# Performance work log

Hardware: AMD Instinct MI355X
Metric: run time of the kernel (lower is better)

Reference implementation:

```python
import jax, jax.numpy as jnp
import numpy as np

B, C, N, T = 16, 32, 1024, 128
R = 10  # low-rank bottleneck of W1/W2


def setup_inputs() -> dict:
    key = jax.random.key(0)
    k1, k2, k3, k4 = jax.random.split(key, 4)
    x = jax.random.normal(k1, (B, C, N, T), dtype=jnp.float32)
    W1 = jax.random.normal(k2, (R, N), dtype=jnp.float32) * 0.05
    W2 = jax.random.normal(k3, (R, N), dtype=jnp.float32) * 0.05
    alpha = jax.random.normal(k4, (C,), dtype=jnp.float32) * 0.1
    return {"x": x, "W1": W1, "W2": W2, "alpha": alpha}


def reference(x, W1, W2, alpha):
    # k = q = einsum('bint,i->btn', x, alpha): contract channels -> [B, T, N]
    k = jnp.einsum('bcnt,c->btn', x, alpha)
    # low-rank bilinear scores: (k @ W1^T) @ (k @ W2^T)^T -> [B, T, T]
    kw1 = jnp.einsum('btn,rn->btr', k, W1)   # [B, T, R]
    qw2 = jnp.einsum('btn,rn->btr', k, W2)   # [B, T, R]
    scores = jnp.einsum('btr,bsr->bts', kw1, qw2)  # [B, T, T]
    att = jax.nn.softmax(scores, axis=-1)
    # weighted sum over time: einsum('bti,bcni->bcnt', att, x)
    return jnp.einsum('bts,bcns->bcnt', att, x)
```

## Files before the change

### kernel.cpp

```cpp
#include <hip/hip_runtime.h>
#include <hip/hip_bf16.h>


#define B_ 16
#define C_ 32
#define N_ 1024
#define T_ 128
#define R_ 10
#define CH_ 16
#define NCH_ (N_ / CH_)

typedef __bf16 bf16x8 __attribute__((ext_vector_type(8)));
typedef __bf16 bf16x4 __attribute__((ext_vector_type(4)));
typedef float f32x4 __attribute__((ext_vector_type(4)));

__global__ __launch_bounds__(256) void k_reduce_c(const float* __restrict__ x,
                                                  const float* __restrict__ alpha,
                                                  float* __restrict__ k) {
    int bid = blockIdx.x;
    int b   = bid >> 7;
    int nc  = bid & 127;
    int tid = threadIdx.x;
    int nl  = tid >> 5;
    int lc  = tid & 31;
    int n   = nc * 8 + nl;
    const float4* xb = reinterpret_cast<const float4*>(
        x + ((size_t)(b * C_) * N_ + n) * T_) + lc;
    float4 acc = {0.f, 0.f, 0.f, 0.f};
    #pragma unroll 8
    for (int c = 0; c < C_; ++c) {
        float a = alpha[c];
        float4 v = xb[(size_t)c * (N_ * T_ / 4)];
        acc.x += a * v.x; acc.y += a * v.y; acc.z += a * v.z; acc.w += a * v.w;
    }
    reinterpret_cast<float4*>(k + ((size_t)b * N_ + n) * T_)[lc] = acc;
}

__global__ __launch_bounds__(128) void kw_partial(const float* __restrict__ k,
                                                  const float* __restrict__ W1,
                                                  const float* __restrict__ W2,
                                                  float* __restrict__ p1,
                                                  float* __restrict__ p2) {
    __shared__ __align__(16) float ws[NCH_][20];
    int bid = blockIdx.x;
    int b   = bid >> 4;
    int ch  = bid & (CH_ - 1);
    int n0  = ch * NCH_;
    int t   = threadIdx.x;
    for (int i = t; i < NCH_ * R_; i += 128) {
        int r = i / NCH_, nl = i % NCH_;
        ws[nl][r]      = W1[r * N_ + n0 + nl];
        ws[nl][R_ + r] = W2[r * N_ + n0 + nl];
    }
    __syncthreads();
    float a1[R_] = {}, a2[R_] = {};
    const float* kb = k + ((size_t)b * N_ + n0) * T_ + t;
    for (int nl = 0; nl < NCH_; ++nl) {
        float kv = kb[nl * T_];
        float wv[20];
        const float4* wr = reinterpret_cast<const float4*>(&ws[nl][0]);
        #pragma unroll
        for (int q = 0; q < 5; ++q) *reinterpret_cast<float4*>(&wv[q * 4]) = wr[q];
        #pragma unroll
        for (int r = 0; r < R_; ++r) {
            a1[r] += kv * wv[r];
            a2[r] += kv * wv[R_ + r];
        }
    }
    size_t o = ((size_t)(b * CH_ + ch) * T_ + t) * R_;
    #pragma unroll
    for (int r = 0; r < R_; ++r) { p1[o + r] = a1[r]; p2[o + r] = a2[r]; }
}

__global__ __launch_bounds__(128) void scores_softmax(const float* __restrict__ p1,
                                                      const float* __restrict__ p2,
                                                      __bf16* __restrict__ att) {
    __shared__ __align__(16) float kw1s[T_][12];
    __shared__ __align__(16) float kw2s[T_][12];
    __shared__ float sc[T_][T_ + 1];
    int b = blockIdx.x;
    int t = threadIdx.x;
    #pragma unroll
    for (int r = 0; r < R_; ++r) {
        float s1 = 0.f, s2 = 0.f;
        for (int ch = 0; ch < CH_; ++ch) {
            size_t o = ((size_t)(b * CH_ + ch) * T_ + t) * R_ + r;
            s1 += p1[o]; s2 += p2[o];
        }
        kw1s[t][r] = s1; kw2s[t][r] = s2;
    }
    __syncthreads();
    float myw[R_];
    #pragma unroll
    for (int r = 0; r < R_; ++r) myw[r] = kw1s[t][r];
    float mx = -1e30f;
    for (int s = 0; s < T_; ++s) {
        float wv[12];
        const float4* qr = reinterpret_cast<const float4*>(&kw2s[s][0]);
        #pragma unroll
        for (int q = 0; q < 3; ++q) *reinterpret_cast<float4*>(&wv[q * 4]) = qr[q];
        float v = 0.f;
        #pragma unroll
        for (int r = 0; r < R_; ++r) v += myw[r] * wv[r];
        sc[t][s] = v;
        mx = fmaxf(mx, v);
    }
    float sum = 0.f;
    for (int s = 0; s < T_; ++s) {
        float e = __expf(sc[t][s] - mx);
        sc[t][s] = e;
        sum += e;
    }
    float inv = 1.0f / sum;
    __bf16* arow = att + ((size_t)b * T_ + t) * T_;
    for (int s8 = 0; s8 < T_; s8 += 8) {
        bf16x8 h;
        #pragma unroll
        for (int q = 0; q < 8; ++q) h[q] = (__bf16)(sc[t][s8 + q] * inv);
        *reinterpret_cast<bf16x8*>(arow + s8) = h;
    }
}

__global__ __launch_bounds__(256) void out_gemm(const float* __restrict__ x,
                                                const __bf16* __restrict__ att,
                                                float* __restrict__ out) {
    __shared__ __align__(16) __bf16 attl[T_][T_];
    __shared__ __align__(16) __bf16 xsl[64][T_];
    int bid = blockIdx.x;
    int nc  = bid & 15;
    int c   = (bid >> 4) & 31;
    int b   = bid >> 9;
    int tid = threadIdx.x;
    size_t slab = ((size_t)(b * C_ + c) * N_ + nc * 64) * T_;
    char* attb = reinterpret_cast<char*>(&attl[0][0]);
    char* xb   = reinterpret_cast<char*>(&xsl[0][0]);

    const uint4* ga = reinterpret_cast<const uint4*>(att + (size_t)b * T_ * T_);
    #pragma unroll
    for (int i = 0; i < 8; ++i) {
        int e   = i * 256 + tid;
        int row = e >> 4;
        int bc  = ((e & 15) * 16) ^ ((row & 7) << 4);
        *reinterpret_cast<uint4*>(attb + row * 256 + bc) = ga[e];
    }
    const float4* gx = reinterpret_cast<const float4*>(x + slab);
    #pragma unroll
    for (int i = 0; i < 8; ++i) {
        int e   = i * 256 + tid;
        int row = e >> 5;
        float4 v = gx[e];
        bf16x4 h = {(__bf16)v.x, (__bf16)v.y, (__bf16)v.z, (__bf16)v.w};
        int bc = ((e & 31) * 8) ^ ((row & 7) << 4);
        *reinterpret_cast<bf16x4*>(xb + row * 256 + bc) = h;
    }
    __syncthreads();

    int wave = tid >> 6, lane = tid & 63;
    int r16 = lane & 15, g = lane >> 4;
    int wt = wave & 1, wn = wave >> 1;
    int swz = (r16 & 7) << 4;
    f32x4 acc[2][4] = {};
    #pragma unroll
    for (int ks = 0; ks < 4; ++ks) {
        int kc = ks * 64 + g * 16;
        bf16x8 a[4], bx[2];
        #pragma unroll
        for (int tt = 0; tt < 4; ++tt) {
            int row = wt * 64 + tt * 16 + r16;
            a[tt] = *reinterpret_cast<const bf16x8*>(attb + row * 256 + (kc ^ swz));
        }
        #pragma unroll
        for (int nn = 0; nn < 2; ++nn) {
            int row = wn * 32 + nn * 16 + r16;
            bx[nn] = *reinterpret_cast<const bf16x8*>(xb + row * 256 + (kc ^ swz));
        }
        #pragma unroll
        for (int nn = 0; nn < 2; ++nn)
            #pragma unroll
            for (int tt = 0; tt < 4; ++tt)
                acc[nn][tt] = __builtin_amdgcn_mfma_f32_16x16x32_bf16(
                    a[tt], bx[nn], acc[nn][tt], 0, 0, 0);
    }
    float* o = out + slab;
    #pragma unroll
    for (int nn = 0; nn < 2; ++nn) {
        int n_l = wn * 32 + nn * 16 + r16;
        #pragma unroll
        for (int tt = 0; tt < 4; ++tt) {
            int t_l = wt * 64 + tt * 16 + g * 4;
            *reinterpret_cast<f32x4*>(o + (size_t)n_l * T_ + t_l) = acc[nn][tt];
        }
    }
}

extern "C" void kernel_launch(void* const* d_in, const int* in_sizes, int n_in,
                              void* d_out, int out_size, void* d_ws, size_t ws_size,
                              hipStream_t stream) {
    const float* x     = (const float*)d_in[0];
    const float* W1    = (const float*)d_in[1];
    const float* W2    = (const float*)d_in[2];
    const float* alpha = (const float*)d_in[3];
    float* out = (float*)d_out;

    float* k  = (float*)d_ws;
    float* p1 = k + (size_t)B_ * N_ * T_;
    float* p2 = p1 + (size_t)B_ * CH_ * T_ * R_;
    __bf16* att = (__bf16*)(p2 + (size_t)B_ * CH_ * T_ * R_);

    k_reduce_c<<<dim3(B_ * (N_ / 8)), dim3(256), 0, stream>>>(x, alpha, k);
    kw_partial<<<dim3(B_ * CH_), dim3(128), 0, stream>>>(k, W1, W2, p1, p2);
    scores_softmax<<<dim3(B_), dim3(128), 0, stream>>>(p1, p2, att);
    out_gemm<<<dim3(B_ * C_ * (N_ / 64)), dim3(256), 0, stream>>>(x, att, out);
}
```

Before: 190.4 us.

## Fuse channel reduction and bf16 cast of x, pipeline output GEMM over slabs

A new first kernel reads x once and does three jobs: it reduces over channels, computes the low-rank projection partials, and writes a swizzled bf16 copy of x into the workspace. The output GEMM then streams that bf16 copy instead of re-reading and converting fp32 x. Each GEMM block handles 8 slabs with double-buffered LDS prefetch and keeps the attention tile loaded across them. This removes the k intermediate and one launch, but adds a 128MB bf16 write. The fused kernel also runs far fewer blocks, and the new path is only taken when the workspace is large enough.

```diff
diff --git a/kernel.cpp b/kernel.cpp
--- a/kernel.cpp
+++ b/kernel.cpp
@@ -13,19 +13,220 @@
 typedef __bf16 bf16x8 __attribute__((ext_vector_type(8)));
 typedef __bf16 bf16x4 __attribute__((ext_vector_type(4)));
 typedef float f32x4 __attribute__((ext_vector_type(4)));
+typedef float f32x2 __attribute__((ext_vector_type(2)));
+
+__global__ __launch_bounds__(256) void k_cast_kw(const float* __restrict__ x,
+                                                 const float* __restrict__ W1,
+                                                 const float* __restrict__ W2,
+                                                 const float* __restrict__ alpha,
+                                                 __bf16* __restrict__ xb16,
+                                                 float* __restrict__ p1,
+                                                 float* __restrict__ p2) {
+    __shared__ float klds[64][T_];
+    __shared__ __align__(16) float wl[64][24];
+    int bid = blockIdx.x;
+    int h   = bid & 1;
+    int nc  = (bid >> 1) & 15;
+    int b   = bid >> 5;
+    int n0  = nc * 64, c0 = h * 16;
+    int tid = threadIdx.x;
+
+    for (int i = tid; i < 64 * 20; i += 256) {
+        int nl = i & 63, q = i >> 6;
+        wl[nl][q < 10 ? q : q + 2] =
+            (q < 10) ? W1[q * N_ + n0 + nl] : W2[(q - 10) * N_ + n0 + nl];
+    }
+    float al[16];
+    #pragma unroll
+    for (int c = 0; c < 16; ++c) al[c] = alpha[c0 + c];
+
+    int col = tid & 31;
+    f32x4 acc[8] = {};
+    const float* xbase = x + (((size_t)b * C_ + c0) * N_ + n0) * T_;
+    #pragma unroll 2
+    for (int cc = 0; cc < 16; ++cc) {
+        const float4* gx = reinterpret_cast<const float4*>(xbase + (size_t)cc * N_ * T_);
+        char* xw = (char*)xb16 + (((size_t)(b * C_ + c0 + cc) * 16 + nc) * 16384);
+        #pragma unroll
+        for (int j = 0; j < 8; ++j) {
+            float4 v = gx[tid + j * 256];
+            int row = (tid >> 5) + j * 8;
+            float a = al[cc];
+            acc[j][0] += a * v.x; acc[j][1] += a * v.y;
+            acc[j][2] += a * v.z; acc[j][3] += a * v.w;
+            bf16x4 hv = {(__bf16)v.x, (__bf16)v.y, (__bf16)v.z, (__bf16)v.w};
+            *reinterpret_cast<bf16x4*>(xw + row * 256 + ((col * 8) ^ ((row & 7) << 4))) = hv;
+        }
+    }
+    #pragma unroll
+    for (int j = 0; j < 8; ++j) {
+        int row = (tid >> 5) + j * 8;
+        *reinterpret_cast<f32x4*>(&klds[row][col * 4]) = acc[j];
+    }
+    __syncthreads();
+    int t = tid & 127, rg = tid >> 7;
+    float a[10] = {};
+    #pragma unroll 4
+    for (int n = 0; n < 64; ++n) {
+        float kv = klds[n][t];
+        const float* wr = &wl[n][rg * 12];
+        f32x4 wA = *reinterpret_cast<const f32x4*>(wr);
+        f32x4 wB = *reinterpret_cast<const f32x4*>(wr + 4);
+        f32x2 wC = *reinterpret_cast<const f32x2*>(wr + 8);
+        a[0] += kv * wA[0]; a[1] += kv * wA[1]; a[2] += kv * wA[2]; a[3] += kv * wA[3];
+        a[4] += kv * wB[0]; a[5] += kv * wB[1]; a[6] += kv * wB[2]; a[7] += kv * wB[3];
+        a[8] += kv * wC[0]; a[9] += kv * wC[1];
+    }
+    float* pd = (rg ? p2 : p1) + (((size_t)b * 32 + (bid & 31)) * T_ + t) * R_;
+    #pragma unroll
+    for (int q = 0; q < 5; ++q) {
+        f32x2 v = {a[2 * q], a[2 * q + 1]};
+        *reinterpret_cast<f32x2*>(pd + 2 * q) = v;
+    }
+}
+
+__global__ __launch_bounds__(128) void scores_softmax32(const float* __restrict__ p1,
+                                                        const float* __restrict__ p2,
+                                                        __bf16* __restrict__ att) {
+    __shared__ __align__(16) float kw1s[T_][12];
+    __shared__ __align__(16) float kw2s[T_][12];
+    __shared__ float sc[T_][T_ + 1];
+    int b = blockIdx.x;
+    int t = threadIdx.x;
+    #pragma unroll
+    for (int r = 0; r < R_; ++r) {
+        float s1 = 0.f, s2 = 0.f;
+        for (int ch = 0; ch < 32; ++ch) {
+            size_t o = (((size_t)b * 32 + ch) * T_ + t) * R_ + r;
+            s1 += p1[o]; s2 += p2[o];
+        }
+        kw1s[t][r] = s1; kw2s[t][r] = s2;
+    }
+    __syncthreads();
+    float myw[R_];
+    #pragma unroll
+    for (int r = 0; r < R_; ++r) myw[r] = kw1s[t][r];
+    float mx = -1e30f;
+    for (int s = 0; s < T_; ++s) {
+        float wv[12];
+        const float4* qr = reinterpret_cast<const float4*>(&kw2s[s][0]);
+        #pragma unroll
+        for (int q = 0; q < 3; ++q) *reinterpret_cast<float4*>(&wv[q * 4]) = qr[q];
+        float v = 0.f;
+        #pragma unroll
+        for (int r = 0; r < R_; ++r) v += myw[r] * wv[r];
+        sc[t][s] = v;
+        mx = fmaxf(mx, v);
+    }
+    float sum = 0.f;
+    for (int s = 0; s < T_; ++s) {
+        float e = __expf(sc[t][s] - mx);
+        sc[t][s] = e;
+        sum += e;
+    }
+    float inv = 1.0f / sum;
+    __bf16* arow = att + ((size_t)b * T_ + t) * T_;
+    for (int s8 = 0; s8 < T_; s8 += 8) {
+        bf16x8 hv;
+        #pragma unroll
+        for (int q = 0; q < 8; ++q) hv[q] = (__bf16)(sc[t][s8 + q] * inv);
+        *reinterpret_cast<bf16x8*>(arow + s8) = hv;
+    }
+}
+
+__global__ __launch_bounds__(256) void out_gemm_p(const __bf16* __restrict__ xb16,
+                                                  const __bf16* __restrict__ att,
+                                                  float* __restrict__ out) {
+    __shared__ __align__(16) __bf16 attl[T_][T_];
+    __shared__ __align__(16) __bf16 xbuf[2][64][T_];
+    int bid = blockIdx.x;
+    int b = bid >> 6, j = bid & 63;
+    int tid = threadIdx.x;
+    char* attb = (char*)&attl[0][0];
+
+    const uint4* ga = reinterpret_cast<const uint4*>(att + (size_t)b * T_ * T_);
+    uint4 ar[8];
+    #pragma unroll
+    for (int i = 0; i < 8; ++i) ar[i] = ga[i * 256 + tid];
+    const uint4* gx0 = reinterpret_cast<const uint4*>(xb16) + ((size_t)b * 512 + (size_t)j * 8) * 1024;
+    uint4 xr[4];
+    #pragma unroll
+    for (int q = 0; q < 4; ++q) xr[q] = gx0[q * 256 + tid];
+    #pragma unroll
+    for (int i = 0; i < 8; ++i) {
+        int e = i * 256 + tid, row = e >> 4;
+        int bc = ((e & 15) * 16) ^ ((row & 7) << 4);
+        *reinterpret_cast<uint4*>(attb + row * 256 + bc) = ar[i];
+    }
+    {
+        uint4* lb = reinterpret_cast<uint4*>(&xbuf[0][0][0]);
+        #pragma unroll
+        for (int q = 0; q < 4; ++q) lb[q * 256 + tid] = xr[q];
+    }
+    __syncthreads();
+
+    int wave = tid >> 6, lane = tid & 63;
+    int r16 = lane & 15, g = lane >> 4;
+    int wt = wave & 1, wn = wave >> 1;
+    int swz = (r16 & 7) << 4;
+
+    for (int i = 0; i < 8; ++i) {
+        int cur = i & 1;
+        uint4 nx[4];
+        if (i < 7) {
+            const uint4* gx = reinterpret_cast<const uint4*>(xb16) +
+                              ((size_t)b * 512 + (size_t)j * 8 + i + 1) * 1024;
+            #pragma unroll
+            for (int q = 0; q < 4; ++q) nx[q] = gx[q * 256 + tid];
+        }
+        const char* xb = (const char*)&xbuf[cur][0][0];
+        f32x4 acc[2][4] = {};
+        #pragma unroll
+        for (int ks = 0; ks < 4; ++ks) {
+            int kc = ks * 64 + g * 16;
+            bf16x8 a[4], bx[2];
+            #pragma unroll
+            for (int tt = 0; tt < 4; ++tt)
+                a[tt] = *reinterpret_cast<const bf16x8*>(
+                    attb + (wt * 64 + tt * 16 + r16) * 256 + (kc ^ swz));
+            #pragma unroll
+            for (int nn = 0; nn < 2; ++nn)
+                bx[nn] = *reinterpret_cast<const bf16x8*>(
+                    xb + (wn * 32 + nn * 16 + r16) * 256 + (kc ^ swz));
+            #pragma unroll
+            for (int nn = 0; nn < 2; ++nn)
+                #pragma unroll
+                for (int tt = 0; tt < 4; ++tt)
+                    acc[nn][tt] = __builtin_amdgcn_mfma_f32_16x16x32_bf16(
+                        a[tt], bx[nn], acc[nn][tt], 0, 0, 0);
+        }
+        int sid = j * 8 + i;
+        float* o = out + (((size_t)(b * C_ + (sid >> 4))) * N_ + (sid & 15) * 64) * T_;
+        #pragma unroll
+        for (int nn = 0; nn < 2; ++nn) {
+            int n_l = wn * 32 + nn * 16 + r16;
+            #pragma unroll
+            for (int tt = 0; tt < 4; ++tt)
+                *reinterpret_cast<f32x4*>(o + (size_t)n_l * T_ + (wt * 64 + tt * 16 + g * 4)) = acc[nn][tt];
+        }
+        if (i < 7) {
+            uint4* lb = reinterpret_cast<uint4*>(&xbuf[cur ^ 1][0][0]);
+            #pragma unroll
+            for (int q = 0; q < 4; ++q) lb[q * 256 + tid] = nx[q];
+        }
+        __syncthreads();
+    }
+}
 
 __global__ __launch_bounds__(256) void k_reduce_c(const float* __restrict__ x,
                                                   const float* __restrict__ alpha,
                                                   float* __restrict__ k) {
     int bid = blockIdx.x;
-    int b   = bid >> 7;
-    int nc  = bid & 127;
+    int b = bid >> 7, nc = bid & 127;
     int tid = threadIdx.x;
-    int nl  = tid >> 5;
-    int lc  = tid & 31;
-    int n   = nc * 8 + nl;
-    const float4* xb = reinterpret_cast<const float4*>(
-        x + ((size_t)(b * C_) * N_ + n) * T_) + lc;
+    int nl = tid >> 5, lc = tid & 31;
+    int n = nc * 8 + nl;
+    const float4* xb = reinterpret_cast<const float4*>(x + ((size_t)(b * C_) * N_ + n) * T_) + lc;
     float4 acc = {0.f, 0.f, 0.f, 0.f};
     #pragma unroll 8
     for (int c = 0; c < C_; ++c) {
@@ -43,28 +244,24 @@
                                                   float* __restrict__ p2) {
     __shared__ __align__(16) float ws[NCH_][20];
     int bid = blockIdx.x;
-    int b   = bid >> 4;
-    int ch  = bid & (CH_ - 1);
-    int n0  = ch * NCH_;
-    int t   = threadIdx.x;
+    int b = bid >> 4, ch = bid & (CH_ - 1);
+    int n0 = ch * NCH_;
+    int t = threadIdx.x;
     for (int i = t; i < NCH_ * R_; i += 128) {
         int r = i / NCH_, nl = i % NCH_;
-        ws[nl][r]      = W1[r * N_ + n0 + nl];
+        ws[nl][r] = W1[r * N_ + n0 + nl];
         ws[nl][R_ + r] = W2[r * N_ + n0 + nl];
     }
     __syncthreads();
     float a1[R_] = {}, a2[R_] = {};
     const float* kb = k + ((size_t)b * N_ + n0) * T_ + t;
+    #pragma unroll 4
     for (int nl = 0; nl < NCH_; ++nl) {
         float kv = kb[nl * T_];
-        float wv[20];
-        const float4* wr = reinterpret_cast<const float4*>(&ws[nl][0]);
-        #pragma unroll
-        for (int q = 0; q < 5; ++q) *reinterpret_cast<float4*>(&wv[q * 4]) = wr[q];
         #pragma unroll
         for (int r = 0; r < R_; ++r) {
-            a1[r] += kv * wv[r];
-            a2[r] += kv * wv[R_ + r];
+            a1[r] += kv * ws[nl][r];
+            a2[r] += kv * ws[nl][R_ + r];
         }
     }
     size_t o = ((size_t)(b * CH_ + ch) * T_ + t) * R_;
@@ -72,9 +269,9 @@
     for (int r = 0; r < R_; ++r) { p1[o + r] = a1[r]; p2[o + r] = a2[r]; }
 }
 
-__global__ __launch_bounds__(128) void scores_softmax(const float* __restrict__ p1,
-                                                      const float* __restrict__ p2,
-                                                      __bf16* __restrict__ att) {
+__global__ __launch_bounds__(128) void scores_softmax16(const float* __restrict__ p1,
+                                                        const float* __restrict__ p2,
+                                                        __bf16* __restrict__ att) {
     __shared__ __align__(16) float kw1s[T_][12];
     __shared__ __align__(16) float kw2s[T_][12];
     __shared__ float sc[T_][T_ + 1];
@@ -95,13 +292,9 @@
     for (int r = 0; r < R_; ++r) myw[r] = kw1s[t][r];
     float mx = -1e30f;
     for (int s = 0; s < T_; ++s) {
-        float wv[12];
-        const float4* qr = reinterpret_cast<const float4*>(&kw2s[s][0]);
-        #pragma unroll
-        for (int q = 0; q < 3; ++q) *reinterpret_cast<float4*>(&wv[q * 4]) = qr[q];
         float v = 0.f;
         #pragma unroll
-        for (int r = 0; r < R_; ++r) v += myw[r] * wv[r];
+        for (int r = 0; r < R_; ++r) v += myw[r] * kw2s[s][r];
         sc[t][s] = v;
         mx = fmaxf(mx, v);
     }
@@ -114,10 +307,10 @@
     float inv = 1.0f / sum;
     __bf16* arow = att + ((size_t)b * T_ + t) * T_;
     for (int s8 = 0; s8 < T_; s8 += 8) {
-        bf16x8 h;
-        #pragma unroll
-        for (int q = 0; q < 8; ++q) h[q] = (__bf16)(sc[t][s8 + q] * inv);
-        *reinterpret_cast<bf16x8*>(arow + s8) = h;
+        bf16x8 hv;
+        #pragma unroll
+        for (int q = 0; q < 8; ++q) hv[q] = (__bf16)(sc[t][s8 + q] * inv);
+        *reinterpret_cast<bf16x8*>(arow + s8) = hv;
     }
 }
 
@@ -127,34 +320,28 @@
     __shared__ __align__(16) __bf16 attl[T_][T_];
     __shared__ __align__(16) __bf16 xsl[64][T_];
     int bid = blockIdx.x;
-    int nc  = bid & 15;
-    int c   = (bid >> 4) & 31;
-    int b   = bid >> 9;
+    int nc = bid & 15, c = (bid >> 4) & 31, b = bid >> 9;
     int tid = threadIdx.x;
     size_t slab = ((size_t)(b * C_ + c) * N_ + nc * 64) * T_;
     char* attb = reinterpret_cast<char*>(&attl[0][0]);
-    char* xb   = reinterpret_cast<char*>(&xsl[0][0]);
-
+    char* xb = reinterpret_cast<char*>(&xsl[0][0]);
     const uint4* ga = reinterpret_cast<const uint4*>(att + (size_t)b * T_ * T_);
     #pragma unroll
     for (int i = 0; i < 8; ++i) {
-        int e   = i * 256 + tid;
-        int row = e >> 4;
-        int bc  = ((e & 15) * 16) ^ ((row & 7) << 4);
+        int e = i * 256 + tid, row = e >> 4;
+        int bc = ((e & 15) * 16) ^ ((row & 7) << 4);
         *reinterpret_cast<uint4*>(attb + row * 256 + bc) = ga[e];
     }
     const float4* gx = reinterpret_cast<const float4*>(x + slab);
     #pragma unroll
     for (int i = 0; i < 8; ++i) {
-        int e   = i * 256 + tid;
-        int row = e >> 5;
+        int e = i * 256 + tid, row = e >> 5;
         float4 v = gx[e];
-        bf16x4 h = {(__bf16)v.x, (__bf16)v.y, (__bf16)v.z, (__bf16)v.w};
+        bf16x4 hv = {(__bf16)v.x, (__bf16)v.y, (__bf16)v.z, (__bf16)v.w};
         int bc = ((e & 31) * 8) ^ ((row & 7) << 4);
-        *reinterpret_cast<bf16x4*>(xb + row * 256 + bc) = h;
-    }
-    __syncthreads();
-
+        *reinterpret_cast<bf16x4*>(xb + row * 256 + bc) = hv;
+    }
+    __syncthreads();
     int wave = tid >> 6, lane = tid & 63;
     int r16 = lane & 15, g = lane >> 4;
     int wt = wave & 1, wn = wave >> 1;
@@ -165,31 +352,24 @@
         int kc = ks * 64 + g * 16;
         bf16x8 a[4], bx[2];
         #pragma unroll
-        for (int tt = 0; tt < 4; ++tt) {
-            int row = wt * 64 + tt * 16 + r16;
-            a[tt] = *reinterpret_cast<const bf16x8*>(attb + row * 256 + (kc ^ swz));
-        }
-        #pragma unroll
-        for (int nn = 0; nn < 2; ++nn) {
-            int row = wn * 32 + nn * 16 + r16;
-            bx[nn] = *reinterpret_cast<const bf16x8*>(xb + row * 256 + (kc ^ swz));
-        }
+        for (int tt = 0; tt < 4; ++tt)
+            a[tt] = *reinterpret_cast<const bf16x8*>(attb + (wt * 64 + tt * 16 + r16) * 256 + (kc ^ swz));
         #pragma unroll
         for (int nn = 0; nn < 2; ++nn)
+            bx[nn] = *reinterpret_cast<const bf16x8*>(xb + (wn * 32 + nn * 16 + r16) * 256 + (kc ^ swz));
+        #pragma unroll
+        for (int nn = 0; nn < 2; ++nn)
             #pragma unroll
             for (int tt = 0; tt < 4; ++tt)
-                acc[nn][tt] = __builtin_amdgcn_mfma_f32_16x16x32_bf16(
-                    a[tt], bx[nn], acc[nn][tt], 0, 0, 0);
+                acc[nn][tt] = __builtin_amdgcn_mfma_f32_16x16x32_bf16(a[tt], bx[nn], acc[nn][tt], 0, 0, 0);
     }
     float* o = out + slab;
     #pragma unroll
     for (int nn = 0; nn < 2; ++nn) {
         int n_l = wn * 32 + nn * 16 + r16;
         #pragma unroll
-        for (int tt = 0; tt < 4; ++tt) {
-            int t_l = wt * 64 + tt * 16 + g * 4;
-            *reinterpret_cast<f32x4*>(o + (size_t)n_l * T_ + t_l) = acc[nn][tt];
-        }
+        for (int tt = 0; tt < 4; ++tt)
+            *reinterpret_cast<f32x4*>(o + (size_t)n_l * T_ + (wt * 64 + tt * 16 + g * 4)) = acc[nn][tt];
     }
 }
 
@@ -202,13 +382,24 @@
     const float* alpha = (const float*)d_in[3];
     float* out = (float*)d_out;
 
-    float* k  = (float*)d_ws;
-    float* p1 = k + (size_t)B_ * N_ * T_;
-    float* p2 = p1 + (size_t)B_ * CH_ * T_ * R_;
-    __bf16* att = (__bf16*)(p2 + (size_t)B_ * CH_ * T_ * R_);
-
-    k_reduce_c<<<dim3(B_ * (N_ / 8)), dim3(256), 0, stream>>>(x, alpha, k);
-    kw_partial<<<dim3(B_ * CH_), dim3(128), 0, stream>>>(k, W1, W2, p1, p2);
-    scores_softmax<<<dim3(B_), dim3(128), 0, stream>>>(p1, p2, att);
-    out_gemm<<<dim3(B_ * C_ * (N_ / 64)), dim3(256), 0, stream>>>(x, att, out);
-}
+    const size_t XB16 = 134217728;
+    const size_t PSZ  = 2621440;
+    if (ws_size >= XB16 + 2 * PSZ + 524288) {
+        __bf16* xb16 = (__bf16*)d_ws;
+        float* p1 = (float*)((char*)d_ws + XB16);
+        float* p2 = (float*)((char*)d_ws + XB16 + PSZ);
+        __bf16* att = (__bf16*)((char*)d_ws + XB16 + 2 * PSZ);
+        k_cast_kw<<<dim3(B_ * 32), dim3(256), 0, stream>>>(x, W1, W2, alpha, xb16, p1, p2);
+        scores_softmax32<<<dim3(B_), dim3(128), 0, stream>>>(p1, p2, att);
+        out_gemm_p<<<dim3(B_ * 64), dim3(256), 0, stream>>>(xb16, att, out);
+    } else {
+        float* k  = (float*)d_ws;
+        float* p1 = k + (size_t)B_ * N_ * T_;
+        float* p2 = p1 + (size_t)B_ * CH_ * T_ * R_;
+        __bf16* att = (__bf16*)(p2 + (size_t)B_ * CH_ * T_ * R_);
+        k_reduce_c<<<dim3(B_ * (N_ / 8)), dim3(256), 0, stream>>>(x, alpha, k);
+        kw_partial<<<dim3(B_ * CH_), dim3(128), 0, stream>>>(k, W1, W2, p1, p2);
+        scores_softmax16<<<dim3(B_), dim3(128), 0, stream>>>(p1, p2, att);
+        out_gemm<<<dim3(B_ * C_ * (N_ / 64)), dim3(256), 0, stream>>>(x, att, out);
+    }
+}
```

Measured after the change: 215.6 us. +13.2%, slower.

## Fuse scores/softmax into output GEMM and split low-rank projection reduction

Applied to the files above, without the earlier changes.

Every output GEMM block now recomputes its batch's scores and softmax in shared memory from the reduced low-rank projections, so the bf16 attention matrix no longer goes through global memory and the 16-block scores_softmax kernel (with its single-block-per-batch serial tail) is gone. Normalisation is deferred to the GEMM epilogue by scaling with 1/sum. The projection partials are split into 32 chunks with a coalesced layout and summed by a separate reduce kernel. The cost is redundant score computation across the 512 blocks per batch, plus extra shared-memory and register pressure in the GEMM kernel.

```diff
diff --git a/kernel.cpp b/kernel.cpp
--- a/kernel.cpp
+++ b/kernel.cpp
@@ -7,12 +7,11 @@
 #define N_ 1024
 #define T_ 128
 #define R_ 10
-#define CH_ 16
-#define NCH_ (N_ / CH_)
 
 typedef __bf16 bf16x8 __attribute__((ext_vector_type(8)));
 typedef __bf16 bf16x4 __attribute__((ext_vector_type(4)));
 typedef float f32x4 __attribute__((ext_vector_type(4)));
+typedef float f32x2 __attribute__((ext_vector_type(2)));
 
 __global__ __launch_bounds__(256) void k_reduce_c(const float* __restrict__ x,
                                                   const float* __restrict__ alpha,
@@ -36,122 +35,148 @@
     reinterpret_cast<float4*>(k + ((size_t)b * N_ + n) * T_)[lc] = acc;
 }
 
-__global__ __launch_bounds__(128) void kw_partial(const float* __restrict__ k,
-                                                  const float* __restrict__ W1,
-                                                  const float* __restrict__ W2,
-                                                  float* __restrict__ p1,
-                                                  float* __restrict__ p2) {
-    __shared__ __align__(16) float ws[NCH_][20];
-    int bid = blockIdx.x;
-    int b   = bid >> 4;
-    int ch  = bid & (CH_ - 1);
-    int n0  = ch * NCH_;
+__global__ __launch_bounds__(128) void kw_partial2(const float* __restrict__ k,
+                                                   const float* __restrict__ W1,
+                                                   const float* __restrict__ W2,
+                                                   float* __restrict__ p1,
+                                                   float* __restrict__ p2) {
+    __shared__ float wl[32][20];
+    int bid = blockIdx.x;
+    int b   = bid >> 5;
+    int ch  = bid & 31;
+    int n0  = ch * 32;
     int t   = threadIdx.x;
-    for (int i = t; i < NCH_ * R_; i += 128) {
-        int r = i / NCH_, nl = i % NCH_;
-        ws[nl][r]      = W1[r * N_ + n0 + nl];
-        ws[nl][R_ + r] = W2[r * N_ + n0 + nl];
+    for (int i = t; i < 32 * 20; i += 128) {
+        int nl = i & 31, q = i >> 5;
+        wl[nl][q] = (q < 10) ? W1[q * N_ + n0 + nl] : W2[(q - 10) * N_ + n0 + nl];
     }
     __syncthreads();
     float a1[R_] = {}, a2[R_] = {};
     const float* kb = k + ((size_t)b * N_ + n0) * T_ + t;
-    for (int nl = 0; nl < NCH_; ++nl) {
-        float kv = kb[nl * T_];
-        float wv[20];
-        const float4* wr = reinterpret_cast<const float4*>(&ws[nl][0]);
-        #pragma unroll
-        for (int q = 0; q < 5; ++q) *reinterpret_cast<float4*>(&wv[q * 4]) = wr[q];
-        #pragma unroll
-        for (int r = 0; r < R_; ++r) {
-            a1[r] += kv * wv[r];
-            a2[r] += kv * wv[R_ + r];
+    #pragma unroll 2
+    for (int g = 0; g < 4; ++g) {
+        float kv[8];
+        #pragma unroll
+        for (int j = 0; j < 8; ++j) kv[j] = kb[(g * 8 + j) * T_];
+        #pragma unroll
+        for (int j = 0; j < 8; ++j) {
+            int nl = g * 8 + j;
+            #pragma unroll
+            for (int r = 0; r < R_; ++r) {
+                a1[r] += kv[j] * wl[nl][r];
+                a2[r] += kv[j] * wl[nl][10 + r];
+            }
         }
     }
-    size_t o = ((size_t)(b * CH_ + ch) * T_ + t) * R_;
-    #pragma unroll
-    for (int r = 0; r < R_; ++r) { p1[o + r] = a1[r]; p2[o + r] = a2[r]; }
-}
-
-__global__ __launch_bounds__(128) void scores_softmax(const float* __restrict__ p1,
-                                                      const float* __restrict__ p2,
-                                                      __bf16* __restrict__ att) {
-    __shared__ __align__(16) float kw1s[T_][12];
-    __shared__ __align__(16) float kw2s[T_][12];
-    __shared__ float sc[T_][T_ + 1];
-    int b = blockIdx.x;
+    #pragma unroll
+    for (int r = 0; r < R_; ++r) {
+        size_t o = (((size_t)b * R_ + r) * 32 + ch) * T_ + t;
+        p1[o] = a1[r];
+        p2[o] = a2[r];
+    }
+}
+
+__global__ __launch_bounds__(128) void kw_reduce(const float* __restrict__ p1,
+                                                 const float* __restrict__ p2,
+                                                 float* __restrict__ kwc) {
+    int bid = blockIdx.x;
+    int b = bid / 20;
+    int q = bid - b * 20;
+    int w = q / 10;
+    int r = q - w * 10;
     int t = threadIdx.x;
-    #pragma unroll
-    for (int r = 0; r < R_; ++r) {
-        float s1 = 0.f, s2 = 0.f;
-        for (int ch = 0; ch < CH_; ++ch) {
-            size_t o = ((size_t)(b * CH_ + ch) * T_ + t) * R_ + r;
-            s1 += p1[o]; s2 += p2[o];
-        }
-        kw1s[t][r] = s1; kw2s[t][r] = s2;
-    }
-    __syncthreads();
-    float myw[R_];
-    #pragma unroll
-    for (int r = 0; r < R_; ++r) myw[r] = kw1s[t][r];
-    float mx = -1e30f;
-    for (int s = 0; s < T_; ++s) {
-        float wv[12];
-        const float4* qr = reinterpret_cast<const float4*>(&kw2s[s][0]);
-        #pragma unroll
-        for (int q = 0; q < 3; ++q) *reinterpret_cast<float4*>(&wv[q * 4]) = qr[q];
-        float v = 0.f;
-        #pragma unroll
-        for (int r = 0; r < R_; ++r) v += myw[r] * wv[r];
-        sc[t][s] = v;
-        mx = fmaxf(mx, v);
-    }
-    float sum = 0.f;
-    for (int s = 0; s < T_; ++s) {
-        float e = __expf(sc[t][s] - mx);
-        sc[t][s] = e;
-        sum += e;
-    }
-    float inv = 1.0f / sum;
-    __bf16* arow = att + ((size_t)b * T_ + t) * T_;
-    for (int s8 = 0; s8 < T_; s8 += 8) {
-        bf16x8 h;
-        #pragma unroll
-        for (int q = 0; q < 8; ++q) h[q] = (__bf16)(sc[t][s8 + q] * inv);
-        *reinterpret_cast<bf16x8*>(arow + s8) = h;
-    }
-}
-
-__global__ __launch_bounds__(256) void out_gemm(const float* __restrict__ x,
-                                                const __bf16* __restrict__ att,
-                                                float* __restrict__ out) {
+    const float* src = (w ? p2 : p1) + (((size_t)b * R_ + r) * 32) * T_ + t;
+    float s = 0.f;
+    #pragma unroll
+    for (int ch = 0; ch < 32; ++ch) s += src[ch * T_];
+    kwc[(((size_t)b * 2 + w) * R_ + r) * T_ + t] = s;
+}
+
+__global__ __launch_bounds__(256) void softmax_gemm(const float* __restrict__ x,
+                                                    const float* __restrict__ kwc,
+                                                    float* __restrict__ out) {
     __shared__ __align__(16) __bf16 attl[T_][T_];
     __shared__ __align__(16) __bf16 xsl[64][T_];
+    __shared__ float invs[T_];
     int bid = blockIdx.x;
     int nc  = bid & 15;
     int c   = (bid >> 4) & 31;
     int b   = bid >> 9;
     int tid = threadIdx.x;
     size_t slab = ((size_t)(b * C_ + c) * N_ + nc * 64) * T_;
-    char* attb = reinterpret_cast<char*>(&attl[0][0]);
-    char* xb   = reinterpret_cast<char*>(&xsl[0][0]);
-
-    const uint4* ga = reinterpret_cast<const uint4*>(att + (size_t)b * T_ * T_);
+    char*  attb = (char*)&attl[0][0];
+    float* kws  = (float*)&xsl[0][0];
+
+    const float* kb = kwc + (size_t)b * 2560;
+    float kwreg[10];
+    #pragma unroll
+    for (int i = 0; i < 10; ++i) kwreg[i] = kb[i * 256 + tid];
+    const float4* gx = reinterpret_cast<const float4*>(x + slab);
+    float4 xr[8];
+    #pragma unroll
+    for (int i = 0; i < 8; ++i) xr[i] = gx[i * 256 + tid];
+    #pragma unroll
+    for (int i = 0; i < 10; ++i) {
+        int idx = i * 256 + tid;
+        int w   = idx >= 1280;
+        int rem = idx - w * 1280;
+        int r   = rem >> 7, t0 = rem & 127;
+        kws[(w * 128 + t0) * 12 + r] = kwreg[i];
+    }
+    __syncthreads();
+
+    int t = tid >> 1, h = tid & 1;
+    const float* w1r = &kws[t * 12];
+    f32x4 m1a = *reinterpret_cast<const f32x4*>(w1r);
+    f32x4 m1b = *reinterpret_cast<const f32x4*>(w1r + 4);
+    f32x2 m1c = *reinterpret_cast<const f32x2*>(w1r + 8);
+    const float* w2base = &kws[(128 + h * 64) * 12];
+    float mx = -1e30f;
+    #pragma unroll 4
+    for (int j = 0; j < 64; ++j) {
+        const float* w2 = w2base + j * 12;
+        f32x4 qa = *reinterpret_cast<const f32x4*>(w2);
+        f32x4 qb = *reinterpret_cast<const f32x4*>(w2 + 4);
+        f32x2 qc = *reinterpret_cast<const f32x2*>(w2 + 8);
+        float v = m1a[0]*qa[0]+m1a[1]*qa[1]+m1a[2]*qa[2]+m1a[3]*qa[3]
+                + m1b[0]*qb[0]+m1b[1]*qb[1]+m1b[2]*qb[2]+m1b[3]*qb[3]
+                + m1c[0]*qc[0]+m1c[1]*qc[1];
+        mx = fmaxf(mx, v);
+    }
+    mx = fmaxf(mx, __shfl_xor(mx, 1));
+    float sum = 0.f;
+    int swzt = (t & 7) << 4;
+    char* arow = attb + t * 256;
+    #pragma unroll 4
+    for (int j = 0; j < 32; ++j) {
+        float v[2];
+        #pragma unroll
+        for (int u = 0; u < 2; ++u) {
+            const float* w2 = w2base + (2 * j + u) * 12;
+            f32x4 qa = *reinterpret_cast<const f32x4*>(w2);
+            f32x4 qb = *reinterpret_cast<const f32x4*>(w2 + 4);
+            f32x2 qc = *reinterpret_cast<const f32x2*>(w2 + 8);
+            v[u] = m1a[0]*qa[0]+m1a[1]*qa[1]+m1a[2]*qa[2]+m1a[3]*qa[3]
+                 + m1b[0]*qb[0]+m1b[1]*qb[1]+m1b[2]*qb[2]+m1b[3]*qb[3]
+                 + m1c[0]*qc[0]+m1c[1]*qc[1];
+        }
+        float e0 = __expf(v[0] - mx), e1 = __expf(v[1] - mx);
+        sum += e0 + e1;
+        union { __bf16 hh[2]; unsigned u32; } cv;
+        cv.hh[0] = (__bf16)e0; cv.hh[1] = (__bf16)e1;
+        int bytec = (h * 128 + j * 4) ^ swzt;
+        *reinterpret_cast<unsigned*>(arow + bytec) = cv.u32;
+    }
+    sum += __shfl_xor(sum, 1);
+    if (h == 0) invs[t] = 1.0f / sum;
+    __syncthreads();
+
+    char* xbb = (char*)&xsl[0][0];
     #pragma unroll
     for (int i = 0; i < 8; ++i) {
-        int e   = i * 256 + tid;
-        int row = e >> 4;
-        int bc  = ((e & 15) * 16) ^ ((row & 7) << 4);
-        *reinterpret_cast<uint4*>(attb + row * 256 + bc) = ga[e];
-    }
-    const float4* gx = reinterpret_cast<const float4*>(x + slab);
-    #pragma unroll
-    for (int i = 0; i < 8; ++i) {
-        int e   = i * 256 + tid;
-        int row = e >> 5;
-        float4 v = gx[e];
-        bf16x4 h = {(__bf16)v.x, (__bf16)v.y, (__bf16)v.z, (__bf16)v.w};
-        int bc = ((e & 31) * 8) ^ ((row & 7) << 4);
-        *reinterpret_cast<bf16x4*>(xb + row * 256 + bc) = h;
+        int e = i * 256 + tid, row = e >> 5;
+        bf16x4 hv = {(__bf16)xr[i].x, (__bf16)xr[i].y, (__bf16)xr[i].z, (__bf16)xr[i].w};
+        *reinterpret_cast<bf16x4*>(xbb + row * 256 + (((e & 31) * 8) ^ ((row & 7) << 4))) = hv;
     }
     __syncthreads();
 
@@ -165,15 +190,13 @@
         int kc = ks * 64 + g * 16;
         bf16x8 a[4], bx[2];
         #pragma unroll
-        for (int tt = 0; tt < 4; ++tt) {
-            int row = wt * 64 + tt * 16 + r16;
-            a[tt] = *reinterpret_cast<const bf16x8*>(attb + row * 256 + (kc ^ swz));
-        }
-        #pragma unroll
-        for (int nn = 0; nn < 2; ++nn) {
-            int row = wn * 32 + nn * 16 + r16;
-            bx[nn] = *reinterpret_cast<const bf16x8*>(xb + row * 256 + (kc ^ swz));
-        }
+        for (int tt = 0; tt < 4; ++tt)
+            a[tt] = *reinterpret_cast<const bf16x8*>(
+                attb + (wt * 64 + tt * 16 + r16) * 256 + (kc ^ swz));
+        #pragma unroll
+        for (int nn = 0; nn < 2; ++nn)
+            bx[nn] = *reinterpret_cast<const bf16x8*>(
+                xbb + (wn * 32 + nn * 16 + r16) * 256 + (kc ^ swz));
         #pragma unroll
         for (int nn = 0; nn < 2; ++nn)
             #pragma unroll
@@ -187,8 +210,11 @@
         int n_l = wn * 32 + nn * 16 + r16;
         #pragma unroll
         for (int tt = 0; tt < 4; ++tt) {
-            int t_l = wt * 64 + tt * 16 + g * 4;
-            *reinterpret_cast<f32x4*>(o + (size_t)n_l * T_ + t_l) = acc[nn][tt];
+            int tb = wt * 64 + tt * 16 + g * 4;
+            f32x4 iv = *reinterpret_cast<const f32x4*>(&invs[tb]);
+            f32x4 vv = acc[nn][tt];
+            vv[0] *= iv[0]; vv[1] *= iv[1]; vv[2] *= iv[2]; vv[3] *= iv[3];
+            *reinterpret_cast<f32x4*>(o + (size_t)n_l * T_ + tb) = vv;
         }
     }
 }
@@ -202,13 +228,13 @@
     const float* alpha = (const float*)d_in[3];
     float* out = (float*)d_out;
 
-    float* k  = (float*)d_ws;
-    float* p1 = k + (size_t)B_ * N_ * T_;
-    float* p2 = p1 + (size_t)B_ * CH_ * T_ * R_;
-    __bf16* att = (__bf16*)(p2 + (size_t)B_ * CH_ * T_ * R_);
-
-    k_reduce_c<<<dim3(B_ * (N_ / 8)), dim3(256), 0, stream>>>(x, alpha, k);
-    kw_partial<<<dim3(B_ * CH_), dim3(128), 0, stream>>>(k, W1, W2, p1, p2);
-    scores_softmax<<<dim3(B_), dim3(128), 0, stream>>>(p1, p2, att);
-    out_gemm<<<dim3(B_ * C_ * (N_ / 64)), dim3(256), 0, stream>>>(x, att, out);
-}
+    float* k   = (float*)d_ws;
+    float* p1  = k  + (size_t)B_ * N_ * T_;
+    float* p2  = p1 + (size_t)B_ * R_ * 32 * T_;
+    float* kwc = p2 + (size_t)B_ * R_ * 32 * T_;
+
+    k_reduce_c <<<dim3(B_ * (N_ / 8)), dim3(256), 0, stream>>>(x, alpha, k);
+    kw_partial2<<<dim3(B_ * 32),       dim3(128), 0, stream>>>(k, W1, W2, p1, p2);
+    kw_reduce  <<<dim3(B_ * 20),       dim3(128), 0, stream>>>(p1, p2, kwc);
+    softmax_gemm<<<dim3(B_ * 512),     dim3(256), 0, stream>>>(x, kwc, out);
+}
```

Measured after the change: 295.2 us. 1.55x slower.

## Load x directly into MFMA registers and parallelize low-rank projection reduction

Applied to the files above, without the earlier changes.

The output GEMM stops staging the x slab through LDS and instead loads fp32 x straight from global memory into registers. It converts those values to bf16 MFMA operands and prefetches the next k-slice, which frees LDS and raises the occupancy hint. The low-rank projection now splits N into 32 chunks with coalesced partial layout. A new small kernel reduces those partials, so scores_softmax no longer serially sums strided partials. This adds a kernel launch, and the direct global loads are less coalesced than the previous staged copy.

```diff
diff --git a/kernel.cpp b/kernel.cpp
--- a/kernel.cpp
+++ b/kernel.cpp
@@ -7,8 +7,6 @@
 #define N_ 1024
 #define T_ 128
 #define R_ 10
-#define CH_ 16
-#define NCH_ (N_ / CH_)
 
 typedef __bf16 bf16x8 __attribute__((ext_vector_type(8)));
 typedef __bf16 bf16x4 __attribute__((ext_vector_type(4)));
@@ -36,58 +34,75 @@
     reinterpret_cast<float4*>(k + ((size_t)b * N_ + n) * T_)[lc] = acc;
 }
 
-__global__ __launch_bounds__(128) void kw_partial(const float* __restrict__ k,
-                                                  const float* __restrict__ W1,
-                                                  const float* __restrict__ W2,
-                                                  float* __restrict__ p1,
-                                                  float* __restrict__ p2) {
-    __shared__ __align__(16) float ws[NCH_][20];
-    int bid = blockIdx.x;
-    int b   = bid >> 4;
-    int ch  = bid & (CH_ - 1);
-    int n0  = ch * NCH_;
+__global__ __launch_bounds__(128) void kw_partial2(const float* __restrict__ k,
+                                                   const float* __restrict__ W1,
+                                                   const float* __restrict__ W2,
+                                                   float* __restrict__ p1,
+                                                   float* __restrict__ p2) {
+    __shared__ float wl[32][20];
+    int bid = blockIdx.x;
+    int b   = bid >> 5;
+    int ch  = bid & 31;
+    int n0  = ch * 32;
     int t   = threadIdx.x;
-    for (int i = t; i < NCH_ * R_; i += 128) {
-        int r = i / NCH_, nl = i % NCH_;
-        ws[nl][r]      = W1[r * N_ + n0 + nl];
-        ws[nl][R_ + r] = W2[r * N_ + n0 + nl];
+    for (int i = t; i < 32 * 20; i += 128) {
+        int nl = i & 31, q = i >> 5;
+        wl[nl][q] = (q < 10) ? W1[q * N_ + n0 + nl] : W2[(q - 10) * N_ + n0 + nl];
     }
     __syncthreads();
     float a1[R_] = {}, a2[R_] = {};
     const float* kb = k + ((size_t)b * N_ + n0) * T_ + t;
-    for (int nl = 0; nl < NCH_; ++nl) {
-        float kv = kb[nl * T_];
-        float wv[20];
-        const float4* wr = reinterpret_cast<const float4*>(&ws[nl][0]);
-        #pragma unroll
-        for (int q = 0; q < 5; ++q) *reinterpret_cast<float4*>(&wv[q * 4]) = wr[q];
-        #pragma unroll
-        for (int r = 0; r < R_; ++r) {
-            a1[r] += kv * wv[r];
-            a2[r] += kv * wv[R_ + r];
+    #pragma unroll 2
+    for (int g = 0; g < 4; ++g) {
+        float kv[8];
+        #pragma unroll
+        for (int j = 0; j < 8; ++j) kv[j] = kb[(g * 8 + j) * T_];
+        #pragma unroll
+        for (int j = 0; j < 8; ++j) {
+            int nl = g * 8 + j;
+            #pragma unroll
+            for (int r = 0; r < R_; ++r) {
+                a1[r] += kv[j] * wl[nl][r];
+                a2[r] += kv[j] * wl[nl][10 + r];
+            }
         }
     }
-    size_t o = ((size_t)(b * CH_ + ch) * T_ + t) * R_;
-    #pragma unroll
-    for (int r = 0; r < R_; ++r) { p1[o + r] = a1[r]; p2[o + r] = a2[r]; }
-}
-
-__global__ __launch_bounds__(128) void scores_softmax(const float* __restrict__ p1,
-                                                      const float* __restrict__ p2,
+    #pragma unroll
+    for (int r = 0; r < R_; ++r) {
+        size_t o = (((size_t)b * R_ + r) * 32 + ch) * T_ + t;
+        p1[o] = a1[r];
+        p2[o] = a2[r];
+    }
+}
+
+__global__ __launch_bounds__(128) void kw_reduce(const float* __restrict__ p1,
+                                                 const float* __restrict__ p2,
+                                                 float* __restrict__ kwc) {
+    int bid = blockIdx.x;
+    int b = bid / 20;
+    int q = bid - b * 20;
+    int w = q / 10;
+    int r = q - w * 10;
+    int t = threadIdx.x;
+    const float* src = (w ? p2 : p1) + (((size_t)b * R_ + r) * 32) * T_ + t;
+    float s = 0.f;
+    #pragma unroll
+    for (int ch = 0; ch < 32; ++ch) s += src[ch * T_];
+    kwc[(((size_t)b * 2 + w) * R_ + r) * T_ + t] = s;
+}
+
+__global__ __launch_bounds__(128) void scores_softmax(const float* __restrict__ kwc,
                                                       __bf16* __restrict__ att) {
     __shared__ __align__(16) float kw1s[T_][12];
     __shared__ __align__(16) float kw2s[T_][12];
     __shared__ float sc[T_][T_ + 1];
     int b = blockIdx.x;
     int t = threadIdx.x;
+    const float* kb = kwc + (size_t)b * 2 * R_ * T_;
     #pragma unroll
     for (int r = 0; r < R_; ++r) {
-        float s1 = 0.f, s2 = 0.f;
-        for (int ch = 0; ch < CH_; ++ch) {
-            size_t o = ((size_t)(b * CH_ + ch) * T_ + t) * R_ + r;
-            s1 += p1[o]; s2 += p2[o];
-        }
-        kw1s[t][r] = s1; kw2s[t][r] = s2;
+        kw1s[t][r] = kb[r * T_ + t];
+        kw2s[t][r] = kb[(R_ + r) * T_ + t];
     }
     __syncthreads();
     float myw[R_];
@@ -114,44 +129,31 @@
     float inv = 1.0f / sum;
     __bf16* arow = att + ((size_t)b * T_ + t) * T_;
     for (int s8 = 0; s8 < T_; s8 += 8) {
-        bf16x8 h;
-        #pragma unroll
-        for (int q = 0; q < 8; ++q) h[q] = (__bf16)(sc[t][s8 + q] * inv);
-        *reinterpret_cast<bf16x8*>(arow + s8) = h;
-    }
-}
-
-__global__ __launch_bounds__(256) void out_gemm(const float* __restrict__ x,
-                                                const __bf16* __restrict__ att,
-                                                float* __restrict__ out) {
+        bf16x8 hv;
+        #pragma unroll
+        for (int q = 0; q < 8; ++q) hv[q] = (__bf16)(sc[t][s8 + q] * inv);
+        *reinterpret_cast<bf16x8*>(arow + s8) = hv;
+    }
+}
+
+__global__ __launch_bounds__(256, 4) void out_gemm2(const float* __restrict__ x,
+                                                    const __bf16* __restrict__ att,
+                                                    float* __restrict__ out) {
     __shared__ __align__(16) __bf16 attl[T_][T_];
-    __shared__ __align__(16) __bf16 xsl[64][T_];
     int bid = blockIdx.x;
     int nc  = bid & 15;
     int c   = (bid >> 4) & 31;
     int b   = bid >> 9;
     int tid = threadIdx.x;
     size_t slab = ((size_t)(b * C_ + c) * N_ + nc * 64) * T_;
-    char* attb = reinterpret_cast<char*>(&attl[0][0]);
-    char* xb   = reinterpret_cast<char*>(&xsl[0][0]);
+    char* attb = (char*)&attl[0][0];
 
     const uint4* ga = reinterpret_cast<const uint4*>(att + (size_t)b * T_ * T_);
     #pragma unroll
     for (int i = 0; i < 8; ++i) {
-        int e   = i * 256 + tid;
-        int row = e >> 4;
-        int bc  = ((e & 15) * 16) ^ ((row & 7) << 4);
+        int e = i * 256 + tid, row = e >> 4;
+        int bc = ((e & 15) * 16) ^ ((row & 7) << 4);
         *reinterpret_cast<uint4*>(attb + row * 256 + bc) = ga[e];
-    }
-    const float4* gx = reinterpret_cast<const float4*>(x + slab);
-    #pragma unroll
-    for (int i = 0; i < 8; ++i) {
-        int e   = i * 256 + tid;
-        int row = e >> 5;
-        float4 v = gx[e];
-        bf16x4 h = {(__bf16)v.x, (__bf16)v.y, (__bf16)v.z, (__bf16)v.w};
-        int bc = ((e & 31) * 8) ^ ((row & 7) << 4);
-        *reinterpret_cast<bf16x4*>(xb + row * 256 + bc) = h;
     }
     __syncthreads();
 
@@ -159,37 +161,50 @@
     int r16 = lane & 15, g = lane >> 4;
     int wt = wave & 1, wn = wave >> 1;
     int swz = (r16 & 7) << 4;
+
+    const float* xr0 = x + slab + (size_t)(wn * 32 + r16) * T_ + g * 8;
+    const float* xr1 = xr0 + 16 * T_;
+
     f32x4 acc[2][4] = {};
+    float4 c0a = *reinterpret_cast<const float4*>(xr0);
+    float4 c0b = *reinterpret_cast<const float4*>(xr0 + 4);
+    float4 c1a = *reinterpret_cast<const float4*>(xr1);
+    float4 c1b = *reinterpret_cast<const float4*>(xr1 + 4);
     #pragma unroll
     for (int ks = 0; ks < 4; ++ks) {
+        float4 n0a, n0b, n1a, n1b;
+        if (ks < 3) {
+            int o = (ks + 1) * 32;
+            n0a = *reinterpret_cast<const float4*>(xr0 + o);
+            n0b = *reinterpret_cast<const float4*>(xr0 + o + 4);
+            n1a = *reinterpret_cast<const float4*>(xr1 + o);
+            n1b = *reinterpret_cast<const float4*>(xr1 + o + 4);
+        }
+        bf16x8 bx0 = {(__bf16)c0a.x, (__bf16)c0a.y, (__bf16)c0a.z, (__bf16)c0a.w,
+                      (__bf16)c0b.x, (__bf16)c0b.y, (__bf16)c0b.z, (__bf16)c0b.w};
+        bf16x8 bx1 = {(__bf16)c1a.x, (__bf16)c1a.y, (__bf16)c1a.z, (__bf16)c1a.w,
+                      (__bf16)c1b.x, (__bf16)c1b.y, (__bf16)c1b.z, (__bf16)c1b.w};
         int kc = ks * 64 + g * 16;
-        bf16x8 a[4], bx[2];
-        #pragma unroll
-        for (int tt = 0; tt < 4; ++tt) {
-            int row = wt * 64 + tt * 16 + r16;
-            a[tt] = *reinterpret_cast<const bf16x8*>(attb + row * 256 + (kc ^ swz));
-        }
-        #pragma unroll
-        for (int nn = 0; nn < 2; ++nn) {
-            int row = wn * 32 + nn * 16 + r16;
-            bx[nn] = *reinterpret_cast<const bf16x8*>(xb + row * 256 + (kc ^ swz));
-        }
-        #pragma unroll
-        for (int nn = 0; nn < 2; ++nn)
-            #pragma unroll
-            for (int tt = 0; tt < 4; ++tt)
-                acc[nn][tt] = __builtin_amdgcn_mfma_f32_16x16x32_bf16(
-                    a[tt], bx[nn], acc[nn][tt], 0, 0, 0);
+        bf16x8 a[4];
+        #pragma unroll
+        for (int tt = 0; tt < 4; ++tt)
+            a[tt] = *reinterpret_cast<const bf16x8*>(
+                attb + (wt * 64 + tt * 16 + r16) * 256 + (kc ^ swz));
+        #pragma unroll
+        for (int tt = 0; tt < 4; ++tt)
+            acc[0][tt] = __builtin_amdgcn_mfma_f32_16x16x32_bf16(a[tt], bx0, acc[0][tt], 0, 0, 0);
+        #pragma unroll
+        for (int tt = 0; tt < 4; ++tt)
+            acc[1][tt] = __builtin_amdgcn_mfma_f32_16x16x32_bf16(a[tt], bx1, acc[1][tt], 0, 0, 0);
+        c0a = n0a; c0b = n0b; c1a = n1a; c1b = n1b;
     }
     float* o = out + slab;
     #pragma unroll
     for (int nn = 0; nn < 2; ++nn) {
         int n_l = wn * 32 + nn * 16 + r16;
         #pragma unroll
-        for (int tt = 0; tt < 4; ++tt) {
-            int t_l = wt * 64 + tt * 16 + g * 4;
-            *reinterpret_cast<f32x4*>(o + (size_t)n_l * T_ + t_l) = acc[nn][tt];
-        }
+        for (int tt = 0; tt < 4; ++tt)
+            *reinterpret_cast<f32x4*>(o + (size_t)n_l * T_ + (wt * 64 + tt * 16 + g * 4)) = acc[nn][tt];
     }
 }
 
@@ -202,13 +217,15 @@
     const float* alpha = (const float*)d_in[3];
     float* out = (float*)d_out;
 
-    float* k  = (float*)d_ws;
-    float* p1 = k + (size_t)B_ * N_ * T_;
-    float* p2 = p1 + (size_t)B_ * CH_ * T_ * R_;
-    __bf16* att = (__bf16*)(p2 + (size_t)B_ * CH_ * T_ * R_);
-
-    k_reduce_c<<<dim3(B_ * (N_ / 8)), dim3(256), 0, stream>>>(x, alpha, k);
-    kw_partial<<<dim3(B_ * CH_), dim3(128), 0, stream>>>(k, W1, W2, p1, p2);
-    scores_softmax<<<dim3(B_), dim3(128), 0, stream>>>(p1, p2, att);
-    out_gemm<<<dim3(B_ * C_ * (N_ / 64)), dim3(256), 0, stream>>>(x, att, out);
-}
+    float* k    = (float*)d_ws;
+    float* p1   = k   + (size_t)B_ * N_ * T_;
+    float* p2   = p1  + (size_t)B_ * R_ * 32 * T_;
+    float* kwc  = p2  + (size_t)B_ * R_ * 32 * T_;
+    __bf16* att = (__bf16*)(kwc + (size_t)B_ * 2 * R_ * T_);
+
+    k_reduce_c   <<<dim3(B_ * (N_ / 8)), dim3(256), 0, stream>>>(x, alpha, k);
+    kw_partial2  <<<dim3(B_ * 32),       dim3(128), 0, stream>>>(k, W1, W2, p1, p2);
+    kw_reduce    <<<dim3(B_ * 20),       dim3(128), 0, stream>>>(p1, p2, kwc);
+    scores_softmax<<<dim3(B_),           dim3(128), 0, stream>>>(kwc, att);
+    out_gemm2    <<<dim3(B_ * 512),      dim3(256), 0, stream>>>(x, att, out);
+}
```

After: 214.3 us. 12.6% more time.
